# Kernel optimization log

Measured on AMD Instinct MI355X. Metric: run time of the kernel, lower is better.

## Reference

```python
import jax, jax.numpy as jnp
import numpy as np
from jax import lax

D_MODEL, D_STATE, D_CONV, EXPAND = 192, 16, 3, 2
D_INNER = EXPAND * D_MODEL          # 384
DT_RANK = -(-D_MODEL // 16)         # 12
LN_EPS = 1e-5


def setup_inputs() -> dict:
    key = jax.random.key(0)
    ks = jax.random.split(key, 12)
    B, H, W = 4, 64, 64
    inv_sq = lambda n: 1.0 / np.sqrt(n)
    x = jax.random.normal(ks[0], (B, H, W, D_MODEL), jnp.float32)
    prompt = jax.random.normal(ks[1], (B, H, W, D_MODEL), jnp.float32)
    W_in = jax.random.normal(ks[2], (D_MODEL, 2 * D_INNER), jnp.float32) * inv_sq(D_MODEL)
    conv_w = jax.random.normal(ks[3], (D_INNER, 1, D_CONV, D_CONV), jnp.float32) * inv_sq(D_CONV * D_CONV)
    conv_b = jax.random.normal(ks[4], (D_INNER,), jnp.float32) * 0.02
    Wx = jax.random.normal(ks[5], (D_INNER, DT_RANK + 2 * D_STATE), jnp.float32) * inv_sq(D_INNER)
    Wdt = jax.random.uniform(ks[6], (DT_RANK, D_INNER), jnp.float32, -DT_RANK ** -0.5, DT_RANK ** -0.5)
    # dt bias init: inverse softplus of dt ~ LogUniform(1e-3, 0.1)
    dt = jnp.exp(jax.random.uniform(ks[7], (D_INNER,), jnp.float32) * (np.log(0.1) - np.log(1e-3)) + np.log(1e-3))
    dt = jnp.clip(dt, 1e-4, None)
    b_dt = dt + jnp.log(-jnp.expm1(-dt))
    A_log = jnp.log(jnp.broadcast_to(jnp.arange(1, D_STATE + 1, dtype=jnp.float32), (D_INNER, D_STATE)))
    D = jnp.ones((D_INNER,), jnp.float32)
    Wp = jax.random.normal(ks[8], (D_MODEL, D_STATE), jnp.float32) * inv_sq(D_MODEL)
    ln_g = jnp.ones((D_INNER,), jnp.float32)
    ln_b = jnp.zeros((D_INNER,), jnp.float32)
    Wout = jax.random.normal(ks[9], (D_INNER, D_MODEL), jnp.float32) * inv_sq(D_INNER)
    return dict(x=x, prompt=prompt, W_in=W_in, conv_w=conv_w, conv_b=conv_b, Wx=Wx,
                Wdt=Wdt, b_dt=b_dt, A_log=A_log, D=D, Wp=Wp, ln_g=ln_g, ln_b=ln_b, Wout=Wout)


def _selective_scan(u, delta, A, Bs, Cs, D):
    # u, delta: [B, L, d]; Bs, Cs: [B, L, n]; A: [d, n]; D: [d]
    Bsz = u.shape[0]
    h0 = jnp.zeros((Bsz, D_INNER, D_STATE), u.dtype)

    def step(h, inp):
        dl, uu, b, c = inp                      # [B,d],[B,d],[B,n],[B,n]
        dA = jnp.exp(dl[..., None] * A)          # [B,d,n]
        h = dA * h + (dl * uu)[..., None] * b[:, None, :]
        y = jnp.einsum('bdn,bn->bd', h, c)
        return h, y

    xs = (jnp.moveaxis(delta, 1, 0), jnp.moveaxis(u, 1, 0),
          jnp.moveaxis(Bs, 1, 0), jnp.moveaxis(Cs, 1, 0))
    _, ys = lax.scan(step, h0, xs)               # ys: [L,B,d]
    return jnp.moveaxis(ys, 0, 1) + u * D        # [B,L,d]


def reference(x, prompt, W_in, conv_w, conv_b, Wx, Wdt, b_dt, A_log, D, Wp, ln_g, ln_b, Wout):
    B, H, W, C = x.shape
    L = H * W
    xz = x @ W_in                                 # [B,H,W,2*d_inner]
    xi, z = jnp.split(xz, 2, axis=-1)
    # depthwise conv2d (NCHW, groups=d_inner)
    xc = jnp.transpose(xi, (0, 3, 1, 2))
    pad = (D_CONV - 1) // 2
    xc = lax.conv_general_dilated(xc, conv_w, (1, 1), [(pad, pad), (pad, pad)],
                                  dimension_numbers=('NCHW', 'OIHW', 'NCHW'),
                                  feature_group_count=D_INNER)
    xc = xc + conv_b[None, :, None, None]
    xc = jax.nn.silu(xc)
    u = jnp.transpose(xc.reshape(B, D_INNER, L), (0, 2, 1))   # [B,L,d]
    x_dbl = u @ Wx                                            # [B,L,r+2n]
    dtr = x_dbl[..., :DT_RANK]
    Bs = x_dbl[..., DT_RANK:DT_RANK + D_STATE]
    Cs = x_dbl[..., DT_RANK + D_STATE:]
    delta = jax.nn.softplus(dtr @ Wdt + b_dt)                 # [B,L,d] (delta_bias + softplus)
    Cs = Cs + prompt.reshape(B, L, C) @ Wp                    # prompt-conditioned C
    A = -jnp.exp(A_log)                                       # [d,n]
    y = _selective_scan(u, delta, A, Bs, Cs, D)               # [B,L,d]
    # out_norm (LayerNorm over d_inner)
    mu = jnp.mean(y, axis=-1, keepdims=True)
    var = jnp.mean(jnp.square(y - mu), axis=-1, keepdims=True)
    y = (y - mu) * lax.rsqrt(var + LN_EPS) * ln_g + ln_b
    y = y.reshape(B, H, W, D_INNER)
    y = y * jax.nn.silu(z)
    return y @ Wout
```

## Files before the change

### kernel.cpp

```cpp
#include <hip/hip_runtime.h>
#include <hip/hip_bf16.h>

#define BB 4
#define HH 64
#define WW 64
#define LL 4096
#define DM 192
#define DI 384
#define NS 16
#define RK 12
#define NC 256
#define CH 16
#define ROWS 16384
#define XDS 64
#define KA 576
#define LOG2E 1.44269504f
#define LN2   0.69314718f

typedef __bf16 bf16x8 __attribute__((ext_vector_type(8)));
typedef float  f32x4  __attribute__((ext_vector_type(4)));

#if defined(__has_builtin)
#if __has_builtin(__builtin_amdgcn_exp2f)
#define fexp2(x) __builtin_amdgcn_exp2f(x)
#else
#define fexp2(x) exp2f(x)
#endif
#else
#define fexp2(x) exp2f(x)
#endif

__device__ __forceinline__ float fsilu(float x) {
    return x / (1.0f + __expf(-x));
}

__device__ __forceinline__ unsigned short f2bf(float f) {
    unsigned int u = __float_as_uint(f);
    unsigned int r = (u + 0x7fffu + ((u >> 16) & 1u)) >> 16;
    return (unsigned short)r;
}
__device__ __forceinline__ float bf2f(unsigned short v) {
    return __uint_as_float((unsigned int)v << 16);
}

__global__ __launch_bounds__(256) void f32_to_bf16_vec(
    const float* __restrict__ src, unsigned short* __restrict__ dst, int n4)
{
    int i = blockIdx.x * 256 + threadIdx.x;
    if (i < n4) {
        float4 v = ((const float4*)src)[i];
        ((ushort4*)dst)[i] = make_ushort4(f2bf(v.x), f2bf(v.y), f2bf(v.z), f2bf(v.w));
    }
}

__global__ __launch_bounds__(256) void prompt_to_across(
    const float* __restrict__ prompt, unsigned short* __restrict__ Across)
{
    int i4 = blockIdx.x * 256 + threadIdx.x;
    if (i4 >= ROWS * (DM / 4)) return;
    int row = i4 / (DM / 4), c4 = i4 % (DM / 4);
    float4 v = ((const float4*)prompt)[i4];
    *(ushort4*)&Across[(size_t)row * KA + DI + c4 * 4] =
        make_ushort4(f2bf(v.x), f2bf(v.y), f2bf(v.z), f2bf(v.w));
}

__global__ __launch_bounds__(256) void build_bt(
    const float* __restrict__ src, unsigned short* __restrict__ dst,
    int K, int Nsrc, int Nrows)
{
    int idx = blockIdx.x * 256 + threadIdx.x;
    if (idx >= Nrows * K) return;
    int n = idx / K, k = idx % K;
    dst[idx] = (n < Nsrc) ? f2bf(src[k * Nsrc + n]) : (unsigned short)0;
}

__global__ __launch_bounds__(256) void build_bxt(
    const float* __restrict__ Wx, const float* __restrict__ Wp,
    unsigned short* __restrict__ dst)
{
    int idx = blockIdx.x * 256 + threadIdx.x;
    if (idx >= XDS * KA) return;
    int n = idx / KA, k = idx % KA;
    float v = 0.f;
    if (k < DI) { if (n < 44) v = Wx[k * 44 + n]; }
    else        { if (n >= 28 && n < 44) v = Wp[(k - DI) * NS + (n - 28)]; }
    dst[idx] = f2bf(v);
}

template<bool SPLIT>
__global__ __launch_bounds__(256) void gemm_bf16_mfma(
    const unsigned short* __restrict__ A, const unsigned short* __restrict__ BT,
    float* __restrict__ C0, unsigned short* __restrict__ C1z,
    int M, int N, int K, int halfN)
{
    __shared__ __align__(16) char lds[64 * 80 * 2];
    char* As = lds;
    char* Bs = lds + 64 * 80;
    const int tid = threadIdx.x;
    const int w = tid >> 6, lane = tid & 63;
    const int wm = w >> 1, wn = w & 1;
    const int row0 = blockIdx.x * 64, col0 = blockIdx.y * 64;
    const int r = tid >> 2, cch = tid & 3;
    const int l15 = lane & 15, k8 = lane >> 4;

    f32x4 acc[2][2] = {};
    for (int k0 = 0; k0 < K; k0 += 32) {
        *(float4*)(As + r * 80 + cch * 16) =
            *(const float4*)(A + (size_t)(row0 + r) * K + k0 + cch * 8);
        *(float4*)(Bs + r * 80 + cch * 16) =
            *(const float4*)(BT + (size_t)(col0 + r) * K + k0 + cch * 8);
        __syncthreads();
        bf16x8 a0 = *(const bf16x8*)(As + (wm * 32 +      l15) * 80 + k8 * 16);
        bf16x8 a1 = *(const bf16x8*)(As + (wm * 32 + 16 + l15) * 80 + k8 * 16);
        bf16x8 b0 = *(const bf16x8*)(Bs + (wn * 32 +      l15) * 80 + k8 * 16);
        bf16x8 b1 = *(const bf16x8*)(Bs + (wn * 32 + 16 + l15) * 80 + k8 * 16);
        acc[0][0] = __builtin_amdgcn_mfma_f32_16x16x32_bf16(a0, b0, acc[0][0], 0, 0, 0);
        acc[0][1] = __builtin_amdgcn_mfma_f32_16x16x32_bf16(a0, b1, acc[0][1], 0, 0, 0);
        acc[1][0] = __builtin_amdgcn_mfma_f32_16x16x32_bf16(a1, b0, acc[1][0], 0, 0, 0);
        acc[1][1] = __builtin_amdgcn_mfma_f32_16x16x32_bf16(a1, b1, acc[1][1], 0, 0, 0);
        __syncthreads();
    }

    if (SPLIT && col0 >= halfN) {
        const int cbase = col0 - halfN;
        #pragma unroll
        for (int fm = 0; fm < 2; ++fm)
            #pragma unroll
            for (int fn = 0; fn < 2; ++fn)
                #pragma unroll
                for (int reg = 0; reg < 4; ++reg) {
                    int row = row0 + wm * 32 + fm * 16 + k8 * 4 + reg;
                    int col = cbase + wn * 32 + fn * 16 + l15;
                    C1z[(size_t)row * halfN + col] = f2bf(acc[fm][fn][reg]);
                }
    } else {
        const int cstride = SPLIT ? halfN : N;
        #pragma unroll
        for (int fm = 0; fm < 2; ++fm)
            #pragma unroll
            for (int fn = 0; fn < 2; ++fn)
                #pragma unroll
                for (int reg = 0; reg < 4; ++reg) {
                    int row = row0 + wm * 32 + fm * 16 + k8 * 4 + reg;
                    int col = col0 + wn * 32 + fn * 16 + l15;
                    C0[(size_t)row * cstride + col] = acc[fm][fn][reg];
                }
    }
}

__global__ __launch_bounds__(256) void conv_dw_silu(
    const float* __restrict__ xi, const float* __restrict__ conv_w,
    const float* __restrict__ conv_b, unsigned short* __restrict__ Across)
{
    int idx = blockIdx.x * 256 + threadIdx.x;
    int c4 = idx % 96;
    int rest = idx / 96;
    int w = rest % WW; rest /= WW;
    int h = rest % HH;
    int b = rest / HH;
    int c = c4 * 4;

    float wgt[4][9];
    #pragma unroll
    for (int q = 0; q < 4; ++q)
        #pragma unroll
        for (int t = 0; t < 9; ++t)
            wgt[q][t] = conv_w[(c + q) * 9 + t];

    float4 acc = *(const float4*)&conv_b[c];
    #pragma unroll
    for (int kh = 0; kh < 3; ++kh) {
        int hh = h + kh - 1;
        if ((unsigned)hh >= HH) continue;
        #pragma unroll
        for (int kw = 0; kw < 3; ++kw) {
            int ww = w + kw - 1;
            if ((unsigned)ww >= WW) continue;
            const float4 xv = *(const float4*)&xi[(((size_t)(b * HH + hh)) * WW + ww) * DI + c];
            int t = kh * 3 + kw;
            acc.x += xv.x * wgt[0][t];
            acc.y += xv.y * wgt[1][t];
            acc.z += xv.z * wgt[2][t];
            acc.w += xv.w * wgt[3][t];
        }
    }
    acc.x = fsilu(acc.x); acc.y = fsilu(acc.y);
    acc.z = fsilu(acc.z); acc.w = fsilu(acc.w);
    size_t off = (((size_t)b * LL) + h * WW + w) * KA + c;
    *(ushort4*)&Across[off] = make_ushort4(f2bf(acc.x), f2bf(acc.y), f2bf(acc.z), f2bf(acc.w));
}

__global__ __launch_bounds__(256) void scan_p1_v5(
    const unsigned short* __restrict__ uA, const float* __restrict__ xdbl,
    const float* __restrict__ A_log, const float* __restrict__ Wdt,
    const float* __restrict__ b_dt, float* __restrict__ AH)
{
    const int g = blockIdx.x * 256 + threadIdx.x;
    const int d = g % DI;
    const int bc = g / DI;
    const int b = bc / NC, c = bc % NC;

    float Adn[NS], h[NS];
    {
        const float4* ap4 = (const float4*)(A_log + d * NS);
        #pragma unroll
        for (int q = 0; q < 4; ++q) {
            const float4 v = ap4[q];
            Adn[q*4+0] = -__expf(v.x) * LOG2E;
            Adn[q*4+1] = -__expf(v.y) * LOG2E;
            Adn[q*4+2] = -__expf(v.z) * LOG2E;
            Adn[q*4+3] = -__expf(v.w) * LOG2E;
        }
    }
    float wdt[RK];
    #pragma unroll
    for (int r = 0; r < RK; ++r) wdt[r] = Wdt[r * DI + d];
    const float bdt = b_dt[d];
    #pragma unroll
    for (int n = 0; n < NS; ++n) h[n] = 0.f;

    const size_t rbase = (size_t)(b * LL + c * CH);
    const unsigned short* up = uA + rbase * KA + d;
    const float* xp = xdbl + rbase * XDS;

    float uu = bf2f(up[0]);
    float4 bb0 = *(const float4*)(xp + 12), bb1 = *(const float4*)(xp + 16);
    float4 bb2 = *(const float4*)(xp + 20), bb3 = *(const float4*)(xp + 24);
    float sdlt = 0.f;

    for (int i = 0; i < CH; ++i) {
        const float* xr = xp + (size_t)i * XDS;
        const float4 t0 = *(const float4*)(xr + 0);
        const float4 t1 = *(const float4*)(xr + 4);
        const float4 t2 = *(const float4*)(xr + 8);
        const float uu_n = bf2f(up[(size_t)(i + 1) * KA]);
        const float* xn = xp + (size_t)(i + 1) * XDS;
        const float4 bn0 = *(const float4*)(xn + 12), bn1 = *(const float4*)(xn + 16);
        const float4 bn2 = *(const float4*)(xn + 20), bn3 = *(const float4*)(xn + 24);

        float t = bdt;
        t += t0.x * wdt[0] + t0.y * wdt[1] + t0.z * wdt[2]  + t0.w * wdt[3];
        t += t1.x * wdt[4] + t1.y * wdt[5] + t1.z * wdt[6]  + t1.w * wdt[7];
        t += t2.x * wdt[8] + t2.y * wdt[9] + t2.z * wdt[10] + t2.w * wdt[11];
        const float dlt = (t > 20.f) ? t : LN2 * __log2f(1.f + fexp2(t * LOG2E));

        const float du = dlt * uu;
        sdlt += dlt;
        const float bs[NS] = {bb0.x, bb0.y, bb0.z, bb0.w, bb1.x, bb1.y, bb1.z, bb1.w,
                              bb2.x, bb2.y, bb2.z, bb2.w, bb3.x, bb3.y, bb3.z, bb3.w};
        #pragma unroll
        for (int n = 0; n < NS; ++n) {
            const float a = fexp2(dlt * Adn[n]);
            h[n] = a * h[n] + du * bs[n];
        }
        uu = uu_n;
        bb0 = bn0; bb1 = bn1; bb2 = bn2; bb3 = bn3;
    }
    float* dst = AH + 2 * (((size_t)bc * DI + d) * NS);
    #pragma unroll
    for (int q = 0; q < 8; ++q) {
        const float ap0 = fexp2(sdlt * Adn[2*q]);
        const float ap1 = fexp2(sdlt * Adn[2*q+1]);
        *(float4*)(dst + 4 * q) = make_float4(ap0, h[2*q], ap1, h[2*q+1]);
    }
}

__global__ __launch_bounds__(256) void scan_p2(float2* __restrict__ AH)
{
    const int gid = blockIdx.x * 256 + threadIdx.x;
    const int dn = gid % (DI * NS);
    const int b  = gid / (DI * NS);
    const size_t base = (size_t)b * NC * DI * NS + dn;
    const size_t cs = (size_t)DI * NS;

    float2 buf[4];
    #pragma unroll
    for (int k = 0; k < 4; ++k) buf[k] = AH[base + (size_t)k * cs];

    float hin = 0.f;
    for (int c = 0; c < NC; c += 4) {
        #pragma unroll
        for (int k = 0; k < 4; ++k) {
            const int cn = (c + k + 4 < NC) ? (c + k + 4) : (NC - 1);
            const float2 nxt = AH[base + (size_t)cn * cs];
            const float2 cur = buf[k];
            AH[base + (size_t)(c + k) * cs].x = hin;
            hin = cur.x * hin + cur.y;
            buf[k] = nxt;
        }
    }
}

__global__ __launch_bounds__(384) void scan_p3_ln_v3(
    const unsigned short* __restrict__ uA, const unsigned short* __restrict__ z_bf,
    const float* __restrict__ xdbl, const float* __restrict__ AH,
    const float* __restrict__ A_log, const float* __restrict__ Wdt,
    const float* __restrict__ b_dt, const float* __restrict__ Dvec,
    const float* __restrict__ ln_g, const float* __restrict__ ln_b,
    unsigned short* __restrict__ yin_bf)
{
    __shared__ float red_s[2][8], red_sq[2][8];
    const int d = threadIdx.x;
    const int bc = blockIdx.x;
    const int b = bc / NC, c = bc % NC;
    const int wid = d >> 6, lane = d & 63;

    float Adn[NS], h[NS];
    {
        const float4* ap4 = (const float4*)(A_log + d * NS);
        #pragma unroll
        for (int q = 0; q < 4; ++q) {
            const float4 v = ap4[q];
            Adn[q*4+0] = -__expf(v.x) * LOG2E;
            Adn[q*4+1] = -__expf(v.y) * LOG2E;
            Adn[q*4+2] = -__expf(v.z) * LOG2E;
            Adn[q*4+3] = -__expf(v.w) * LOG2E;
        }
    }
    float wdt[RK];
    #pragma unroll
    for (int r = 0; r < RK; ++r) wdt[r] = Wdt[r * DI + d];
    const float bdt = b_dt[d];
    {
        const float* hp = AH + 2 * (((size_t)bc * DI + d) * NS);
        #pragma unroll
        for (int q = 0; q < 8; ++q) {
            const float4 v = *(const float4*)(hp + 4 * q);
            h[2*q] = v.x; h[2*q+1] = v.z;
        }
    }
    const float Dd = Dvec[d];
    const float lg = ln_g[d], lb = ln_b[d];

    const size_t rbase = (size_t)(b * LL + c * CH);
    const unsigned short* up = uA + rbase * KA + d;
    const unsigned short* zp = z_bf + rbase * DI + d;
    const float* xp = xdbl + rbase * XDS;
    unsigned short* yp = yin_bf + rbase * DI + d;

    float uu = bf2f(up[0]), zz = bf2f(zp[0]);
    float4 bb0 = *(const float4*)(xp + 12), bb1 = *(const float4*)(xp + 16);
    float4 bb2 = *(const float4*)(xp + 20), bb3 = *(const float4*)(xp + 24);
    float4 cc0 = *(const float4*)(xp + 28), cc1 = *(const float4*)(xp + 32);
    float4 cc2 = *(const float4*)(xp + 36), cc3 = *(const float4*)(xp + 40);

    for (int i = 0; i < CH; ++i) {
        const float* xr = xp + (size_t)i * XDS;
        const float4 t0 = *(const float4*)(xr + 0);
        const float4 t1 = *(const float4*)(xr + 4);
        const float4 t2 = *(const float4*)(xr + 8);
        const float uu_n = bf2f(up[(size_t)(i + 1) * KA]);
        const float zz_n = bf2f(zp[(size_t)(i + 1) * DI]);
        const float* xn = xp + (size_t)(i + 1) * XDS;
        const float4 bn0 = *(const float4*)(xn + 12), bn1 = *(const float4*)(xn + 16);
        const float4 bn2 = *(const float4*)(xn + 20), bn3 = *(const float4*)(xn + 24);
        const float4 cn0 = *(const float4*)(xn + 28), cn1 = *(const float4*)(xn + 32);
        const float4 cn2 = *(const float4*)(xn + 36), cn3 = *(const float4*)(xn + 40);

        float t = bdt;
        t += t0.x * wdt[0] + t0.y * wdt[1] + t0.z * wdt[2]  + t0.w * wdt[3];
        t += t1.x * wdt[4] + t1.y * wdt[5] + t1.z * wdt[6]  + t1.w * wdt[7];
        t += t2.x * wdt[8] + t2.y * wdt[9] + t2.z * wdt[10] + t2.w * wdt[11];
        const float dlt = (t > 20.f) ? t : LN2 * __log2f(1.f + fexp2(t * LOG2E));

        const float du = dlt * uu;
        const float bs[NS] = {bb0.x, bb0.y, bb0.z, bb0.w, bb1.x, bb1.y, bb1.z, bb1.w,
                              bb2.x, bb2.y, bb2.z, bb2.w, bb3.x, bb3.y, bb3.z, bb3.w};
        const float cs[NS] = {cc0.x, cc0.y, cc0.z, cc0.w, cc1.x, cc1.y, cc1.z, cc1.w,
                              cc2.x, cc2.y, cc2.z, cc2.w, cc3.x, cc3.y, cc3.z, cc3.w};
        float acc = uu * Dd;
        #pragma unroll
        for (int n = 0; n < NS; ++n) {
            const float a = fexp2(dlt * Adn[n]);
            h[n] = a * h[n] + du * bs[n];
            acc += h[n] * cs[n];
        }
        float s = acc, sq = acc * acc;
        #pragma unroll
        for (int m = 1; m < 64; m <<= 1) {
            s  += __shfl_xor(s, m);
            sq += __shfl_xor(sq, m);
        }
        const int par = i & 1;
        if (lane == 0) { red_s[par][wid] = s; red_sq[par][wid] = sq; }
        __syncthreads();
        s = red_s[par][0] + red_s[par][1] + red_s[par][2]
          + red_s[par][3] + red_s[par][4] + red_s[par][5];
        sq = red_sq[par][0] + red_sq[par][1] + red_sq[par][2]
           + red_sq[par][3] + red_sq[par][4] + red_sq[par][5];
        const float mu = s * (1.f / DI);
        const float var = sq * (1.f / DI) - mu * mu;
        const float inv = rsqrtf(var + 1e-5f);
        const float yn = (acc - mu) * inv * lg + lb;
        yp[(size_t)i * DI] = f2bf(yn * fsilu(zz));

        uu = uu_n; zz = zz_n;
        bb0 = bn0; bb1 = bn1; bb2 = bn2; bb3 = bn3;
        cc0 = cn0; cc1 = cn1; cc2 = cn2; cc3 = cn3;
    }
}

extern "C" void kernel_launch(void* const* d_in, const int* in_sizes, int n_in,
                              void* d_out, int out_size, void* d_ws, size_t ws_size,
                              hipStream_t stream)
{
    const float* x      = (const float*)d_in[0];
    const float* prompt = (const float*)d_in[1];
    const float* W_in   = (const float*)d_in[2];
    const float* conv_w = (const float*)d_in[3];
    const float* conv_b = (const float*)d_in[4];
    const float* Wx     = (const float*)d_in[5];
    const float* Wdt    = (const float*)d_in[6];
    const float* b_dt   = (const float*)d_in[7];
    const float* A_log  = (const float*)d_in[8];
    const float* Dvec   = (const float*)d_in[9];
    const float* Wp     = (const float*)d_in[10];
    const float* ln_g   = (const float*)d_in[11];
    const float* ln_b   = (const float*)d_in[12];
    const float* Wout   = (const float*)d_in[13];
    float* out = (float*)d_out;

    char* p = (char*)d_ws;
    float* xi = (float*)p;                 p += (size_t)ROWS * DI * 4;
    unsigned short* z_bf = (unsigned short*)p;  p += (size_t)(ROWS + 1) * DI * 2;
    unsigned short* Across = (unsigned short*)p; p += (size_t)(ROWS + 1) * KA * 2;
    float* xdbl = (float*)p;               p += (size_t)(ROWS + 1) * XDS * 4;
    char* ahreg = p;
    float* AH = (float*)p;                 p += (size_t)BB * NC * DI * NS * 8;
    unsigned short* WinT  = (unsigned short*)p;  p += (size_t)(2 * DI) * DM * 2;
    unsigned short* BxT   = (unsigned short*)p;  p += (size_t)XDS * KA * 2;
    unsigned short* WoutT = (unsigned short*)p;  p += (size_t)DM * DI * 2;
    unsigned short* x_bf = (unsigned short*)ahreg;
    unsigned short* yin_bf = (unsigned short*)xi;

    f32_to_bf16_vec<<<(ROWS * DM / 4 + 255) / 256, 256, 0, stream>>>(x, x_bf, ROWS * DM / 4);
    prompt_to_across<<<(ROWS * (DM / 4) + 255) / 256, 256, 0, stream>>>(prompt, Across);
    build_bt<<<(2 * DI * DM + 255) / 256, 256, 0, stream>>>(W_in, WinT, DM, 2 * DI, 2 * DI);
    build_bxt<<<(XDS * KA + 255) / 256, 256, 0, stream>>>(Wx, Wp, BxT);
    build_bt<<<(DM * DI + 255) / 256, 256, 0, stream>>>(Wout, WoutT, DI, DM, DM);

    {
        dim3 g(ROWS / 64, (2 * DI) / 64);
        gemm_bf16_mfma<true><<<g, 256, 0, stream>>>(x_bf, WinT, xi, z_bf, ROWS, 2 * DI, DM, DI);
    }
    conv_dw_silu<<<(BB * HH * WW * 96) / 256, 256, 0, stream>>>(xi, conv_w, conv_b, Across);
    {
        dim3 g(ROWS / 64, 1);
        gemm_bf16_mfma<false><<<g, 256, 0, stream>>>(Across, BxT, xdbl, nullptr, ROWS, XDS, KA, 0);
    }
    scan_p1_v5<<<(BB * NC * DI) / 256, 256, 0, stream>>>(Across, xdbl, A_log, Wdt, b_dt, AH);
    scan_p2<<<(BB * DI * NS) / 256, 256, 0, stream>>>((float2*)AH);
    scan_p3_ln_v3<<<BB * NC, 384, 0, stream>>>(Across, z_bf, xdbl, AH, A_log, Wdt,
                                               b_dt, Dvec, ln_g, ln_b, yin_bf);
    {
        dim3 g(ROWS / 64, DM / 64);
        gemm_bf16_mfma<false><<<g, 256, 0, stream>>>(yin_bf, WoutT, out, nullptr, ROWS, DM, DI, 0);
    }
}
```

Baseline: 279.3 us.

## Fold dt projection into x_proj GEMM, store delta and xi in bf16

Precomputes the combined Wx[:, :12]·Wdt weight so the x_proj GEMM also emits delta (with bias and softplus fused in its epilogue) as bf16. The two scan kernels then read delta instead of recomputing the 12-term dot and softplus per step. The in_proj output xi is stored as bf16 rather than fp32, and scan_p2 writes carry-in states to a separate compact buffer. This trades extra GEMM columns and a new delta buffer for less redundant per-step compute and less traffic, at some bf16 precision loss on xi and delta.

```diff
diff --git a/kernel.cpp b/kernel.cpp
--- a/kernel.cpp
+++ b/kernel.cpp
@@ -14,6 +14,7 @@
 #define ROWS 16384
 #define XDS 64
 #define KA 576
+#define NXE 448
 #define LOG2E 1.44269504f
 #define LN2   0.69314718f
 
@@ -74,23 +75,33 @@
     dst[idx] = (n < Nsrc) ? f2bf(src[k * Nsrc + n]) : (unsigned short)0;
 }
 
-__global__ __launch_bounds__(256) void build_bxt(
+__global__ __launch_bounds__(256) void build_bxt_ext(
     const float* __restrict__ Wx, const float* __restrict__ Wp,
-    unsigned short* __restrict__ dst)
+    const float* __restrict__ Wdt, unsigned short* __restrict__ dst)
 {
     int idx = blockIdx.x * 256 + threadIdx.x;
-    if (idx >= XDS * KA) return;
+    if (idx >= NXE * KA) return;
     int n = idx / KA, k = idx % KA;
     float v = 0.f;
-    if (k < DI) { if (n < 44) v = Wx[k * 44 + n]; }
-    else        { if (n >= 28 && n < 44) v = Wp[(k - DI) * NS + (n - 28)]; }
+    if (n < 64) {
+        if (k < DI) { if (n < 44) v = Wx[k * 44 + n]; }
+        else        { if (n >= 28 && n < 44) v = Wp[(k - DI) * NS + (n - 28)]; }
+    } else {
+        if (k < DI) {
+            const int d = n - 64;
+            #pragma unroll
+            for (int r = 0; r < RK; ++r)
+                v += Wx[k * 44 + r] * Wdt[r * DI + d];
+        }
+    }
     dst[idx] = f2bf(v);
 }
 
-template<bool SPLIT>
+template<int MODE>
 __global__ __launch_bounds__(256) void gemm_bf16_mfma(
     const unsigned short* __restrict__ A, const unsigned short* __restrict__ BT,
-    float* __restrict__ C0, unsigned short* __restrict__ C1z,
+    float* __restrict__ C0, unsigned short* __restrict__ D0,
+    unsigned short* __restrict__ D1, const float* __restrict__ b_dt,
     int M, int N, int K, int halfN)
 {
     __shared__ __align__(16) char lds[64 * 80 * 2];
@@ -121,35 +132,36 @@
         __syncthreads();
     }
 
-    if (SPLIT && col0 >= halfN) {
-        const int cbase = col0 - halfN;
-        #pragma unroll
-        for (int fm = 0; fm < 2; ++fm)
+    #pragma unroll
+    for (int fm = 0; fm < 2; ++fm)
+        #pragma unroll
+        for (int fn = 0; fn < 2; ++fn)
             #pragma unroll
-            for (int fn = 0; fn < 2; ++fn)
-                #pragma unroll
-                for (int reg = 0; reg < 4; ++reg) {
-                    int row = row0 + wm * 32 + fm * 16 + k8 * 4 + reg;
-                    int col = cbase + wn * 32 + fn * 16 + l15;
-                    C1z[(size_t)row * halfN + col] = f2bf(acc[fm][fn][reg]);
+            for (int reg = 0; reg < 4; ++reg) {
+                const int row = row0 + wm * 32 + fm * 16 + k8 * 4 + reg;
+                const int col = col0 + wn * 32 + fn * 16 + l15;
+                const float v = acc[fm][fn][reg];
+                if (MODE == 0) {
+                    C0[(size_t)row * N + col] = v;
+                } else if (MODE == 1) {
+                    if (col < halfN) D0[(size_t)row * halfN + col] = f2bf(v);
+                    else             D1[(size_t)row * halfN + col - halfN] = f2bf(v);
+                } else {
+                    if (col < 64) {
+                        C0[(size_t)row * XDS + col] = v;
+                    } else {
+                        const int d = col - 64;
+                        const float t = v + b_dt[d];
+                        const float dl = (t > 20.f) ? t
+                            : LN2 * __log2f(1.f + fexp2(t * LOG2E));
+                        D0[(size_t)row * DI + d] = f2bf(dl);
+                    }
                 }
-    } else {
-        const int cstride = SPLIT ? halfN : N;
-        #pragma unroll
-        for (int fm = 0; fm < 2; ++fm)
-            #pragma unroll
-            for (int fn = 0; fn < 2; ++fn)
-                #pragma unroll
-                for (int reg = 0; reg < 4; ++reg) {
-                    int row = row0 + wm * 32 + fm * 16 + k8 * 4 + reg;
-                    int col = col0 + wn * 32 + fn * 16 + l15;
-                    C0[(size_t)row * cstride + col] = acc[fm][fn][reg];
-                }
-    }
+            }
 }
 
 __global__ __launch_bounds__(256) void conv_dw_silu(
-    const float* __restrict__ xi, const float* __restrict__ conv_w,
+    const unsigned short* __restrict__ xi_bf, const float* __restrict__ conv_w,
     const float* __restrict__ conv_b, unsigned short* __restrict__ Across)
 {
     int idx = blockIdx.x * 256 + threadIdx.x;
@@ -176,12 +188,13 @@
         for (int kw = 0; kw < 3; ++kw) {
             int ww = w + kw - 1;
             if ((unsigned)ww >= WW) continue;
-            const float4 xv = *(const float4*)&xi[(((size_t)(b * HH + hh)) * WW + ww) * DI + c];
+            const ushort4 xv = *(const ushort4*)
+                &xi_bf[(((size_t)(b * HH + hh)) * WW + ww) * DI + c];
             int t = kh * 3 + kw;
-            acc.x += xv.x * wgt[0][t];
-            acc.y += xv.y * wgt[1][t];
-            acc.z += xv.z * wgt[2][t];
-            acc.w += xv.w * wgt[3][t];
+            acc.x += bf2f(xv.x) * wgt[0][t];
+            acc.y += bf2f(xv.y) * wgt[1][t];
+            acc.z += bf2f(xv.z) * wgt[2][t];
+            acc.w += bf2f(xv.w) * wgt[3][t];
         }
     }
     acc.x = fsilu(acc.x); acc.y = fsilu(acc.y);
@@ -190,15 +203,15 @@
     *(ushort4*)&Across[off] = make_ushort4(f2bf(acc.x), f2bf(acc.y), f2bf(acc.z), f2bf(acc.w));
 }
 
-__global__ __launch_bounds__(256) void scan_p1_v5(
-    const unsigned short* __restrict__ uA, const float* __restrict__ xdbl,
-    const float* __restrict__ A_log, const float* __restrict__ Wdt,
-    const float* __restrict__ b_dt, float* __restrict__ AH)
-{
-    const int g = blockIdx.x * 256 + threadIdx.x;
-    const int d = g % DI;
-    const int bc = g / DI;
+__global__ __launch_bounds__(384) void scan_p1_v8(
+    const unsigned short* __restrict__ uA, const unsigned short* __restrict__ delta_bf,
+    const float* __restrict__ xdbl, const float* __restrict__ A_log,
+    float* __restrict__ AH)
+{
+    const int d = threadIdx.x;
+    const int bc = blockIdx.x;
     const int b = bc / NC, c = bc % NC;
+    const size_t rbase = (size_t)(b * LL + c * CH);
 
     float Adn[NS], h[NS];
     {
@@ -212,37 +225,25 @@
             Adn[q*4+3] = -__expf(v.w) * LOG2E;
         }
     }
-    float wdt[RK];
-    #pragma unroll
-    for (int r = 0; r < RK; ++r) wdt[r] = Wdt[r * DI + d];
-    const float bdt = b_dt[d];
     #pragma unroll
     for (int n = 0; n < NS; ++n) h[n] = 0.f;
 
-    const size_t rbase = (size_t)(b * LL + c * CH);
     const unsigned short* up = uA + rbase * KA + d;
+    const unsigned short* dp = delta_bf + rbase * DI + d;
     const float* xp = xdbl + rbase * XDS;
 
-    float uu = bf2f(up[0]);
+    float uu = bf2f(up[0]), dlt = bf2f(dp[0]);
     float4 bb0 = *(const float4*)(xp + 12), bb1 = *(const float4*)(xp + 16);
     float4 bb2 = *(const float4*)(xp + 20), bb3 = *(const float4*)(xp + 24);
     float sdlt = 0.f;
 
+    #pragma unroll
     for (int i = 0; i < CH; ++i) {
-        const float* xr = xp + (size_t)i * XDS;
-        const float4 t0 = *(const float4*)(xr + 0);
-        const float4 t1 = *(const float4*)(xr + 4);
-        const float4 t2 = *(const float4*)(xr + 8);
-        const float uu_n = bf2f(up[(size_t)(i + 1) * KA]);
+        const float uu_n  = bf2f(up[(size_t)(i + 1) * KA]);
+        const float dlt_n = bf2f(dp[(size_t)(i + 1) * DI]);
         const float* xn = xp + (size_t)(i + 1) * XDS;
         const float4 bn0 = *(const float4*)(xn + 12), bn1 = *(const float4*)(xn + 16);
         const float4 bn2 = *(const float4*)(xn + 20), bn3 = *(const float4*)(xn + 24);
-
-        float t = bdt;
-        t += t0.x * wdt[0] + t0.y * wdt[1] + t0.z * wdt[2]  + t0.w * wdt[3];
-        t += t1.x * wdt[4] + t1.y * wdt[5] + t1.z * wdt[6]  + t1.w * wdt[7];
-        t += t2.x * wdt[8] + t2.y * wdt[9] + t2.z * wdt[10] + t2.w * wdt[11];
-        const float dlt = (t > 20.f) ? t : LN2 * __log2f(1.f + fexp2(t * LOG2E));
 
         const float du = dlt * uu;
         sdlt += dlt;
@@ -253,7 +254,7 @@
             const float a = fexp2(dlt * Adn[n]);
             h[n] = a * h[n] + du * bs[n];
         }
-        uu = uu_n;
+        uu = uu_n; dlt = dlt_n;
         bb0 = bn0; bb1 = bn1; bb2 = bn2; bb3 = bn3;
     }
     float* dst = AH + 2 * (((size_t)bc * DI + d) * NS);
@@ -265,7 +266,8 @@
     }
 }
 
-__global__ __launch_bounds__(256) void scan_p2(float2* __restrict__ AH)
+__global__ __launch_bounds__(256) void scan_p2_v2(
+    const float2* __restrict__ AH, float* __restrict__ Hinc)
 {
     const int gid = blockIdx.x * 256 + threadIdx.x;
     const int dn = gid % (DI * NS);
@@ -284,26 +286,26 @@
             const int cn = (c + k + 4 < NC) ? (c + k + 4) : (NC - 1);
             const float2 nxt = AH[base + (size_t)cn * cs];
             const float2 cur = buf[k];
-            AH[base + (size_t)(c + k) * cs].x = hin;
+            Hinc[base + (size_t)(c + k) * cs] = hin;
             hin = cur.x * hin + cur.y;
             buf[k] = nxt;
         }
     }
 }
 
-__global__ __launch_bounds__(384) void scan_p3_ln_v3(
+__global__ __launch_bounds__(384) void scan_p3_ln_v6(
     const unsigned short* __restrict__ uA, const unsigned short* __restrict__ z_bf,
-    const float* __restrict__ xdbl, const float* __restrict__ AH,
-    const float* __restrict__ A_log, const float* __restrict__ Wdt,
-    const float* __restrict__ b_dt, const float* __restrict__ Dvec,
-    const float* __restrict__ ln_g, const float* __restrict__ ln_b,
-    unsigned short* __restrict__ yin_bf)
+    const unsigned short* __restrict__ delta_bf, const float* __restrict__ xdbl,
+    const float* __restrict__ Hinc, const float* __restrict__ A_log,
+    const float* __restrict__ Dvec, const float* __restrict__ ln_g,
+    const float* __restrict__ ln_b, unsigned short* __restrict__ yin_bf)
 {
     __shared__ float red_s[2][8], red_sq[2][8];
     const int d = threadIdx.x;
     const int bc = blockIdx.x;
     const int b = bc / NC, c = bc % NC;
     const int wid = d >> 6, lane = d & 63;
+    const size_t rbase = (size_t)(b * LL + c * CH);
 
     float Adn[NS], h[NS];
     {
@@ -317,51 +319,39 @@
             Adn[q*4+3] = -__expf(v.w) * LOG2E;
         }
     }
-    float wdt[RK];
-    #pragma unroll
-    for (int r = 0; r < RK; ++r) wdt[r] = Wdt[r * DI + d];
-    const float bdt = b_dt[d];
-    {
-        const float* hp = AH + 2 * (((size_t)bc * DI + d) * NS);
-        #pragma unroll
-        for (int q = 0; q < 8; ++q) {
+    {
+        const float* hp = Hinc + ((size_t)bc * DI + d) * NS;
+        #pragma unroll
+        for (int q = 0; q < 4; ++q) {
             const float4 v = *(const float4*)(hp + 4 * q);
-            h[2*q] = v.x; h[2*q+1] = v.z;
+            h[q*4] = v.x; h[q*4+1] = v.y; h[q*4+2] = v.z; h[q*4+3] = v.w;
         }
     }
     const float Dd = Dvec[d];
     const float lg = ln_g[d], lb = ln_b[d];
 
-    const size_t rbase = (size_t)(b * LL + c * CH);
     const unsigned short* up = uA + rbase * KA + d;
     const unsigned short* zp = z_bf + rbase * DI + d;
+    const unsigned short* dp = delta_bf + rbase * DI + d;
     const float* xp = xdbl + rbase * XDS;
     unsigned short* yp = yin_bf + rbase * DI + d;
 
-    float uu = bf2f(up[0]), zz = bf2f(zp[0]);
+    float uu = bf2f(up[0]), zz = bf2f(zp[0]), dlt = bf2f(dp[0]);
     float4 bb0 = *(const float4*)(xp + 12), bb1 = *(const float4*)(xp + 16);
     float4 bb2 = *(const float4*)(xp + 20), bb3 = *(const float4*)(xp + 24);
     float4 cc0 = *(const float4*)(xp + 28), cc1 = *(const float4*)(xp + 32);
     float4 cc2 = *(const float4*)(xp + 36), cc3 = *(const float4*)(xp + 40);
 
+    #pragma unroll
     for (int i = 0; i < CH; ++i) {
-        const float* xr = xp + (size_t)i * XDS;
-        const float4 t0 = *(const float4*)(xr + 0);
-        const float4 t1 = *(const float4*)(xr + 4);
-        const float4 t2 = *(const float4*)(xr + 8);
-        const float uu_n = bf2f(up[(size_t)(i + 1) * KA]);
-        const float zz_n = bf2f(zp[(size_t)(i + 1) * DI]);
+        const float uu_n  = bf2f(up[(size_t)(i + 1) * KA]);
+        const float zz_n  = bf2f(zp[(size_t)(i + 1) * DI]);
+        const float dlt_n = bf2f(dp[(size_t)(i + 1) * DI]);
         const float* xn = xp + (size_t)(i + 1) * XDS;
         const float4 bn0 = *(const float4*)(xn + 12), bn1 = *(const float4*)(xn + 16);
         const float4 bn2 = *(const float4*)(xn + 20), bn3 = *(const float4*)(xn + 24);
         const float4 cn0 = *(const float4*)(xn + 28), cn1 = *(const float4*)(xn + 32);
         const float4 cn2 = *(const float4*)(xn + 36), cn3 = *(const float4*)(xn + 40);
-
-        float t = bdt;
-        t += t0.x * wdt[0] + t0.y * wdt[1] + t0.z * wdt[2]  + t0.w * wdt[3];
-        t += t1.x * wdt[4] + t1.y * wdt[5] + t1.z * wdt[6]  + t1.w * wdt[7];
-        t += t2.x * wdt[8] + t2.y * wdt[9] + t2.z * wdt[10] + t2.w * wdt[11];
-        const float dlt = (t > 20.f) ? t : LN2 * __log2f(1.f + fexp2(t * LOG2E));
 
         const float du = dlt * uu;
         const float bs[NS] = {bb0.x, bb0.y, bb0.z, bb0.w, bb1.x, bb1.y, bb1.z, bb1.w,
@@ -394,7 +384,7 @@
         const float yn = (acc - mu) * inv * lg + lb;
         yp[(size_t)i * DI] = f2bf(yn * fsilu(zz));
 
-        uu = uu_n; zz = zz_n;
+        uu = uu_n; zz = zz_n; dlt = dlt_n;
         bb0 = bn0; bb1 = bn1; bb2 = bn2; bb3 = bn3;
         cc0 = cn0; cc1 = cn1; cc2 = cn2; cc3 = cn3;
     }
@@ -421,39 +411,44 @@
     float* out = (float*)d_out;
 
     char* p = (char*)d_ws;
-    float* xi = (float*)p;                 p += (size_t)ROWS * DI * 4;
-    unsigned short* z_bf = (unsigned short*)p;  p += (size_t)(ROWS + 1) * DI * 2;
-    unsigned short* Across = (unsigned short*)p; p += (size_t)(ROWS + 1) * KA * 2;
-    float* xdbl = (float*)p;               p += (size_t)(ROWS + 1) * XDS * 4;
+    unsigned short* xi_bf   = (unsigned short*)p; p += (size_t)ROWS * DI * 2;
+    unsigned short* z_bf    = (unsigned short*)p; p += (size_t)(ROWS + 1) * DI * 2;
+    unsigned short* Across  = (unsigned short*)p; p += (size_t)(ROWS + 1) * KA * 2;
+    float*          xdbl    = (float*)p;          p += (size_t)(ROWS + 1) * XDS * 4;
+    unsigned short* delta_bf= (unsigned short*)p; p += (size_t)(ROWS + 1) * DI * 2;
     char* ahreg = p;
-    float* AH = (float*)p;                 p += (size_t)BB * NC * DI * NS * 8;
+    float* AH   = (float*)p;               p += (size_t)BB * NC * DI * NS * 8;
+    float* Hinc = (float*)p;               p += (size_t)BB * NC * DI * NS * 4;
     unsigned short* WinT  = (unsigned short*)p;  p += (size_t)(2 * DI) * DM * 2;
-    unsigned short* BxT   = (unsigned short*)p;  p += (size_t)XDS * KA * 2;
+    unsigned short* BxTE  = (unsigned short*)p;  p += (size_t)NXE * KA * 2;
     unsigned short* WoutT = (unsigned short*)p;  p += (size_t)DM * DI * 2;
     unsigned short* x_bf = (unsigned short*)ahreg;
-    unsigned short* yin_bf = (unsigned short*)xi;
+    unsigned short* yin_bf = xi_bf;
 
     f32_to_bf16_vec<<<(ROWS * DM / 4 + 255) / 256, 256, 0, stream>>>(x, x_bf, ROWS * DM / 4);
     prompt_to_across<<<(ROWS * (DM / 4) + 255) / 256, 256, 0, stream>>>(prompt, Across);
     build_bt<<<(2 * DI * DM + 255) / 256, 256, 0, stream>>>(W_in, WinT, DM, 2 * DI, 2 * DI);
-    build_bxt<<<(XDS * KA + 255) / 256, 256, 0, stream>>>(Wx, Wp, BxT);
+    build_bxt_ext<<<(NXE * KA + 255) / 256, 256, 0, stream>>>(Wx, Wp, Wdt, BxTE);
     build_bt<<<(DM * DI + 255) / 256, 256, 0, stream>>>(Wout, WoutT, DI, DM, DM);
 
     {
         dim3 g(ROWS / 64, (2 * DI) / 64);
-        gemm_bf16_mfma<true><<<g, 256, 0, stream>>>(x_bf, WinT, xi, z_bf, ROWS, 2 * DI, DM, DI);
-    }
-    conv_dw_silu<<<(BB * HH * WW * 96) / 256, 256, 0, stream>>>(xi, conv_w, conv_b, Across);
-    {
-        dim3 g(ROWS / 64, 1);
-        gemm_bf16_mfma<false><<<g, 256, 0, stream>>>(Across, BxT, xdbl, nullptr, ROWS, XDS, KA, 0);
-    }
-    scan_p1_v5<<<(BB * NC * DI) / 256, 256, 0, stream>>>(Across, xdbl, A_log, Wdt, b_dt, AH);
-    scan_p2<<<(BB * DI * NS) / 256, 256, 0, stream>>>((float2*)AH);
-    scan_p3_ln_v3<<<BB * NC, 384, 0, stream>>>(Across, z_bf, xdbl, AH, A_log, Wdt,
-                                               b_dt, Dvec, ln_g, ln_b, yin_bf);
+        gemm_bf16_mfma<1><<<g, 256, 0, stream>>>(x_bf, WinT, nullptr, xi_bf, z_bf,
+                                                 nullptr, ROWS, 2 * DI, DM, DI);
+    }
+    conv_dw_silu<<<(BB * HH * WW * 96) / 256, 256, 0, stream>>>(xi_bf, conv_w, conv_b, Across);
+    {
+        dim3 g(ROWS / 64, NXE / 64);
+        gemm_bf16_mfma<2><<<g, 256, 0, stream>>>(Across, BxTE, xdbl, delta_bf,
+                                                 nullptr, b_dt, ROWS, NXE, KA, 64);
+    }
+    scan_p1_v8<<<BB * NC, 384, 0, stream>>>(Across, delta_bf, xdbl, A_log, AH);
+    scan_p2_v2<<<(BB * DI * NS) / 256, 256, 0, stream>>>((const float2*)AH, Hinc);
+    scan_p3_ln_v6<<<BB * NC, 384, 0, stream>>>(Across, z_bf, delta_bf, xdbl, Hinc,
+                                               A_log, Dvec, ln_g, ln_b, yin_bf);
     {
         dim3 g(ROWS / 64, DM / 64);
-        gemm_bf16_mfma<false><<<g, 256, 0, stream>>>(yin_bf, WoutT, out, nullptr, ROWS, DM, DI, 0);
-    }
-}
+        gemm_bf16_mfma<0><<<g, 256, 0, stream>>>(yin_bf, WoutT, out, nullptr, nullptr,
+                                                 nullptr, ROWS, DM, DI, 0);
+    }
+}
```

After: 271.8 us. 2.7% less time.
